# Performance work log

Hardware: AMD Instinct MI355X
Metric: run time of the kernel (lower is better)

Reference implementation:

```python
import jax, jax.numpy as jnp
import numpy as np

D_MODEL = 1024
N_HEADS = 16
HEAD_DIM = D_MODEL // N_HEADS
B, T = 4, 2048


def setup_inputs() -> dict:
    key = jax.random.key(0)
    ks = jax.random.split(key, 5)
    s = 0.02
    return {
        "x": jax.random.normal(ks[0], (B, T, D_MODEL), dtype=jnp.float32),
        "w_qkv": jax.random.normal(ks[1], (D_MODEL, 3 * D_MODEL), dtype=jnp.float32) * s,
        "b_qkv": jnp.zeros((3 * D_MODEL,), dtype=jnp.float32),
        "w_out": jax.random.normal(ks[2], (D_MODEL, D_MODEL), dtype=jnp.float32) * s,
        "b_out": jnp.zeros((D_MODEL,), dtype=jnp.float32),
    }


def reference(x, w_qkv, b_qkv, w_out, b_out):
    Bx, Tx, C = x.shape
    H, Dh = N_HEADS, HEAD_DIM
    qkv = x @ w_qkv + b_qkv                      # [B,T,3C]
    qkv = qkv.reshape(Bx, Tx, 3, H, Dh)
    q = jnp.transpose(qkv[:, :, 0], (0, 2, 1, 3))  # [B,H,T,Dh]
    k = jnp.transpose(qkv[:, :, 1], (0, 2, 1, 3))
    v = jnp.transpose(qkv[:, :, 2], (0, 2, 1, 3))
    scale = 1.0 / jnp.sqrt(jnp.asarray(Dh, dtype=x.dtype))
    attn = jnp.einsum("bhqd,bhkd->bhqk", q, k) * scale  # [B,H,T,T]
    causal = jnp.tril(jnp.ones((Tx, Tx), dtype=bool))
    attn = jnp.where(causal, attn, jnp.asarray(-jnp.inf, dtype=attn.dtype))
    attn = jax.nn.softmax(attn, axis=-1)
    out = jnp.einsum("bhqk,bhkd->bhqd", attn, v)  # [B,H,T,Dh]
    out = jnp.transpose(out, (0, 2, 1, 3)).reshape(Bx, Tx, C)
    return out @ w_out + b_out
```

## Files before the change

### kernel.cpp

```cpp
#include <hip/hip_runtime.h>
#include <hip/hip_bf16.h>
#include <stdint.h>

#define DM    1024
#define NH    16
#define DH    64
#define BATCH 4
#define SEQ   2048
#define QSCALE 0.18033688011112042f

typedef __attribute__((ext_vector_type(4))) float f32x4;
typedef __attribute__((ext_vector_type(8))) short short8;

__device__ __forceinline__ void async_load16(const void* g, void* l) {
    __builtin_amdgcn_global_load_lds(
        (const __attribute__((address_space(1))) void*)(uintptr_t)g,
        (__attribute__((address_space(3))) void*)(uintptr_t)l,
        16, 0, 0);
}

__global__ __launch_bounds__(256) void k_convert(const float* __restrict__ in,
                                                 __hip_bfloat16* __restrict__ out,
                                                 int n4, int* __restrict__ cnt) {
    if (blockIdx.x == 0 && threadIdx.x == 0) cnt[0] = 0;
    int i = blockIdx.x * 256 + threadIdx.x;
    if (i >= n4) return;
    float4 v = ((const float4*)in)[i];
    union { ushort4 u; __hip_bfloat16 h[4]; } o;
    o.h[0] = __float2bfloat16(v.x);
    o.h[1] = __float2bfloat16(v.y);
    o.h[2] = __float2bfloat16(v.z);
    o.h[3] = __float2bfloat16(v.w);
    ((ushort4*)out)[i] = o.u;
}

__global__ __launch_bounds__(256) void k_transpose(const float* __restrict__ in,
                                                   __hip_bfloat16* __restrict__ out,
                                                   int K, int N) {
    __shared__ float tile[32][33];
    const int n0 = blockIdx.x * 32, k0 = blockIdx.y * 32;
    const int tx = threadIdx.x, ty = threadIdx.y;
#pragma unroll
    for (int i = 0; i < 32; i += 8)
        tile[ty + i][tx] = in[(size_t)(k0 + ty + i) * N + n0 + tx];
    __syncthreads();
#pragma unroll
    for (int i = 0; i < 32; i += 8)
        out[(size_t)(n0 + ty + i) * K + k0 + tx] = __float2bfloat16(tile[tx][ty + i]);
}

__global__ __launch_bounds__(512) void k_gemm_qkv(
    const __hip_bfloat16* __restrict__ A, const __hip_bfloat16* __restrict__ Bt,
    const float* __restrict__ bias,
    __hip_bfloat16* __restrict__ qo, __hip_bfloat16* __restrict__ ko,
    __hip_bfloat16* __restrict__ vto) {
    constexpr int K = 1024;
    constexpr int NT = K / 64;
    __shared__ __align__(16) __hip_bfloat16 As[128 * 64];
    __shared__ __align__(16) __hip_bfloat16 Bs[256 * 64];
    const int tid = threadIdx.x;
    const int lane = tid & 63, wid = tid >> 6;
    const int quad = lane >> 4, c = lane & 15;
    const int m0 = blockIdx.y * 128, n0 = blockIdx.x * 256;
    const int wm = (wid >> 2) * 64, wn = (wid & 3) * 64;
    f32x4 acc[4][4] = {};

    auto stage = [&](int k0) {
#pragma unroll
        for (int i = 0; i < 2; ++i) {
            const int s = tid + i * 512;
            const int r = s >> 3;
            const int g = (s & 7) ^ (r & 7);
            async_load16(A + (size_t)(m0 + r) * K + k0 + g * 8, As + s * 8);
        }
#pragma unroll
        for (int i = 0; i < 4; ++i) {
            const int s = tid + i * 512;
            const int r = s >> 3;
            const int g = (s & 7) ^ (r & 7);
            async_load16(Bt + (size_t)(n0 + r) * K + k0 + g * 8, Bs + s * 8);
        }
    };

    stage(0);
    for (int t = 0; t < NT; ++t) {
        asm volatile("s_waitcnt vmcnt(0)" ::: "memory");
        __builtin_amdgcn_s_barrier();
        short8 af[4][2], bf[4][2];
#pragma unroll
        for (int mt = 0; mt < 4; ++mt) {
            const int R = wm + mt * 16 + c;
#pragma unroll
            for (int kk = 0; kk < 2; ++kk)
                af[mt][kk] = *(const short8*)(As + R * 64 + (((kk * 4 + quad) ^ (R & 7)) * 8));
        }
#pragma unroll
        for (int nt = 0; nt < 4; ++nt) {
            const int R = wn + nt * 16 + c;
#pragma unroll
            for (int kk = 0; kk < 2; ++kk)
                bf[nt][kk] = *(const short8*)(Bs + R * 64 + (((kk * 4 + quad) ^ (R & 7)) * 8));
        }
        asm volatile("s_waitcnt lgkmcnt(0)" ::: "memory");
        __builtin_amdgcn_s_barrier();
        if (t + 1 < NT) stage((t + 1) * 64);
        __builtin_amdgcn_s_setprio(1);
#pragma unroll
        for (int kk = 0; kk < 2; ++kk)
#pragma unroll
            for (int mt = 0; mt < 4; ++mt)
#pragma unroll
                for (int nt = 0; nt < 4; ++nt)
                    acc[mt][nt] = __builtin_amdgcn_mfma_f32_16x16x32_bf16(
                        af[mt][kk], bf[nt][kk], acc[mt][nt], 0, 0, 0);
        __builtin_amdgcn_s_setprio(0);
    }

    const int sel = n0 >> 10;
#pragma unroll
    for (int mt = 0; mt < 4; ++mt) {
        const int t0m = m0 + wm + mt * 16 + quad * 4;
        const int b = t0m >> 11, t0 = t0m & 2047;
#pragma unroll
        for (int nt = 0; nt < 4; ++nt) {
            const int n = n0 + wn + nt * 16 + c;
            const int h = (n & 1023) >> 6, dh = n & 63;
            const int bh = b * 16 + h;
            const float bv = bias[n];
            if (sel == 0) {
#pragma unroll
                for (int r = 0; r < 4; ++r)
                    qo[((size_t)bh * 2048 + t0 + r) * 64 + dh] =
                        __float2bfloat16((acc[mt][nt][r] + bv) * QSCALE);
            } else if (sel == 1) {
#pragma unroll
                for (int r = 0; r < 4; ++r)
                    ko[((size_t)bh * 2048 + t0 + r) * 64 + dh] =
                        __float2bfloat16(acc[mt][nt][r] + bv);
            } else {
                union { ushort4 u; __hip_bfloat16 hh[4]; } pk;
#pragma unroll
                for (int r = 0; r < 4; ++r)
                    pk.hh[r] = __float2bfloat16(acc[mt][nt][r] + bv);
                *(ushort4*)(vto + ((size_t)bh * 64 + dh) * 2048 + t0) = pk.u;
            }
        }
    }
}

__global__ __launch_bounds__(256) void k_attn(
    const __hip_bfloat16* __restrict__ q, const __hip_bfloat16* __restrict__ k,
    const __hip_bfloat16* __restrict__ vt, __hip_bfloat16* __restrict__ y,
    int* __restrict__ cnt) {
    __shared__ __align__(16) __hip_bfloat16 Ks[2][64 * 64];
    __shared__ __align__(16) __hip_bfloat16 Vts[2][64 * 64];
    __shared__ int s_item;
    const int tid = threadIdx.x;
    const int lane = tid & 63, w = tid >> 6;
    const int quad = lane >> 4, c = lane & 15;
    const short one = (short)0x3F80;
    const short8 ones = {one, one, one, one, one, one, one, one};

    for (;;) {
        __syncthreads();
        if (tid == 0) s_item = atomicAdd(cnt, 1);
        __syncthreads();
        const int item = s_item;
        if (item >= 1024) break;
        const int qt = 15 - (item >> 6);
        const int bh = item & 63;
        const int b = bh >> 4, h = bh & 15;
        const int q0 = qt * 128;
        const int qw = q0 + w * 32;
        const int nkt = 2 * qt + 2;
        const size_t kbase0 = (size_t)bh * 2048 * 64;
        const size_t vbase0 = (size_t)bh * 64 * 2048;

        short8 qf[2][2];
#pragma unroll
        for (int j = 0; j < 2; ++j) {
            const __hip_bfloat16* qrow = q + ((size_t)bh * 2048 + qw + j * 16 + c) * 64;
            qf[0][j] = *(const short8*)(qrow + quad * 8);
            qf[1][j] = *(const short8*)(qrow + 32 + quad * 8);
        }

        f32x4 accO[2][4] = {};
        f32x4 accL[2] = {};

        auto stage = [&](int kt, int buf) {
#pragma unroll
            for (int i = 0; i < 2; ++i) {
                const int s = tid + i * 256;
                const int r = s >> 3;
                const int g = (s & 7) ^ (r & 7);
                async_load16(k  + kbase0 + (size_t)(kt * 64 + r) * 64 + g * 8,
                             &Ks[buf][s * 8]);
                async_load16(vt + vbase0 + (size_t)r * 2048 + kt * 64 + g * 8,
                             &Vts[buf][s * 8]);
            }
        };

        stage(0, 0);
        for (int kt = 0; kt < nkt; ++kt) {
            const int buf = kt & 1;
            __syncthreads();
            if (kt + 1 < nkt) stage(kt + 1, buf ^ 1);
            if (kt * 64 > qw + 31) continue;
            const __hip_bfloat16* Kb = Ks[buf];
            const __hip_bfloat16* Vb = Vts[buf];

            short8 kf[4][2];
#pragma unroll
            for (int nt = 0; nt < 4; ++nt) {
                const __hip_bfloat16* kr = Kb + (nt * 16 + c) * 64;
                kf[nt][0] = *(const short8*)(kr + ((quad ^ (c & 7)) * 8));
                kf[nt][1] = *(const short8*)(kr + (((quad + 4) ^ (c & 7)) * 8));
            }

            short8 pf[2][2];
#pragma unroll
            for (int j = 0; j < 2; ++j) {
                f32x4 sj[4];
                __builtin_amdgcn_s_setprio(1);
#pragma unroll
                for (int nt = 0; nt < 4; ++nt) {
                    f32x4 z = {};
                    z      = __builtin_amdgcn_mfma_f32_16x16x32_bf16(kf[nt][0], qf[0][j], z, 0, 0, 0);
                    sj[nt] = __builtin_amdgcn_mfma_f32_16x16x32_bf16(kf[nt][1], qf[1][j], z, 0, 0, 0);
                }
                __builtin_amdgcn_s_setprio(0);
                if (kt * 64 + 63 > qw + j * 16) {
                    const int qg = qw + j * 16 + c;
#pragma unroll
                    for (int nt = 0; nt < 4; ++nt) {
                        const int keyb = kt * 64 + nt * 16 + quad * 4;
#pragma unroll
                        for (int r = 0; r < 4; ++r)
                            if (keyb + r > qg) sj[nt][r] = -1e30f;
                    }
                }
#pragma unroll
                for (int nt = 0; nt < 4; ++nt)
#pragma unroll
                    for (int r = 0; r < 4; ++r)
                        sj[nt][r] = __builtin_amdgcn_exp2f(sj[nt][r]);
                unsigned pk32[4][2];
#pragma unroll
                for (int nt = 0; nt < 4; ++nt) {
                    asm("v_cvt_pk_bf16_f32 %0, %1, %2"
                        : "=v"(pk32[nt][0]) : "v"(sj[nt][0]), "v"(sj[nt][1]));
                    asm("v_cvt_pk_bf16_f32 %0, %1, %2"
                        : "=v"(pk32[nt][1]) : "v"(sj[nt][2]), "v"(sj[nt][3]));
                }
                union U8 { unsigned u[4]; short8 v; } w0, w1;
#pragma unroll
                for (int rr = 0; rr < 2; ++rr) {
                    auto t1 = __builtin_amdgcn_permlane32_swap(pk32[0][rr], pk32[1][rr], false, false);
                    auto t2 = __builtin_amdgcn_permlane16_swap(t1[0], t1[1], false, false);
                    w0.u[rr]     = t2[0];
                    w0.u[2 + rr] = t2[1];
                    t1 = __builtin_amdgcn_permlane32_swap(pk32[2][rr], pk32[3][rr], false, false);
                    t2 = __builtin_amdgcn_permlane16_swap(t1[0], t1[1], false, false);
                    w1.u[rr]     = t2[0];
                    w1.u[2 + rr] = t2[1];
                }
                pf[0][j] = w0.v;
                pf[1][j] = w1.v;
            }

            __builtin_amdgcn_s_setprio(1);
#pragma unroll
            for (int j = 0; j < 2; ++j) {
                accL[j] = __builtin_amdgcn_mfma_f32_16x16x32_bf16(ones, pf[0][j], accL[j], 0, 0, 0);
                accL[j] = __builtin_amdgcn_mfma_f32_16x16x32_bf16(ones, pf[1][j], accL[j], 0, 0, 0);
            }
#pragma unroll
            for (int dt = 0; dt < 4; ++dt) {
                const __hip_bfloat16* vr = Vb + (dt * 16 + c) * 64;
                short8 vf0 = *(const short8*)(vr + ((quad ^ (c & 7)) * 8));
                short8 vf1 = *(const short8*)(vr + (((quad + 4) ^ (c & 7)) * 8));
#pragma unroll
                for (int j = 0; j < 2; ++j) {
                    accO[j][dt] = __builtin_amdgcn_mfma_f32_16x16x32_bf16(vf0, pf[0][j], accO[j][dt], 0, 0, 0);
                    accO[j][dt] = __builtin_amdgcn_mfma_f32_16x16x32_bf16(vf1, pf[1][j], accO[j][dt], 0, 0, 0);
                }
            }
            __builtin_amdgcn_s_setprio(0);
        }
#pragma unroll
        for (int j = 0; j < 2; ++j) {
            const float inv = 1.0f / accL[j][0];
            const int qg = qw + j * 16 + c;
#pragma unroll
            for (int dt = 0; dt < 4; ++dt) {
                union { ushort4 u; __hip_bfloat16 hh[4]; } o;
#pragma unroll
                for (int r = 0; r < 4; ++r)
                    o.hh[r] = __float2bfloat16(accO[j][dt][r] * inv);
                *(ushort4*)(y + ((size_t)b * 2048 + qg) * 1024 + h * 64 + dt * 16 + quad * 4) = o.u;
            }
        }
    }
}

__global__ __launch_bounds__(512) void k_gemm_out(
    const __hip_bfloat16* __restrict__ A, const __hip_bfloat16* __restrict__ Bt,
    const float* __restrict__ bias, float* __restrict__ out) {
    constexpr int K = 1024;
    constexpr int NT = K / 64;
    __shared__ __align__(16) __hip_bfloat16 As[128 * 64];
    __shared__ __align__(16) __hip_bfloat16 Bs[256 * 64];
    const int tid = threadIdx.x;
    const int lane = tid & 63, wid = tid >> 6;
    const int quad = lane >> 4, c = lane & 15;
    const int m0 = blockIdx.y * 128, n0 = blockIdx.x * 256;
    const int wm = (wid >> 2) * 64, wn = (wid & 3) * 64;
    f32x4 acc[4][4] = {};

    auto stage = [&](int k0) {
#pragma unroll
        for (int i = 0; i < 2; ++i) {
            const int s = tid + i * 512;
            const int r = s >> 3;
            const int g = (s & 7) ^ (r & 7);
            async_load16(A + (size_t)(m0 + r) * K + k0 + g * 8, As + s * 8);
        }
#pragma unroll
        for (int i = 0; i < 4; ++i) {
            const int s = tid + i * 512;
            const int r = s >> 3;
            const int g = (s & 7) ^ (r & 7);
            async_load16(Bt + (size_t)(n0 + r) * K + k0 + g * 8, Bs + s * 8);
        }
    };

    stage(0);
    for (int t = 0; t < NT; ++t) {
        asm volatile("s_waitcnt vmcnt(0)" ::: "memory");
        __builtin_amdgcn_s_barrier();
        short8 af[4][2], bf[4][2];
#pragma unroll
        for (int mt = 0; mt < 4; ++mt) {
            const int R = wm + mt * 16 + c;
#pragma unroll
            for (int kk = 0; kk < 2; ++kk)
                af[mt][kk] = *(const short8*)(As + R * 64 + (((kk * 4 + quad) ^ (R & 7)) * 8));
        }
#pragma unroll
        for (int nt = 0; nt < 4; ++nt) {
            const int R = wn + nt * 16 + c;
#pragma unroll
            for (int kk = 0; kk < 2; ++kk)
                bf[nt][kk] = *(const short8*)(Bs + R * 64 + (((kk * 4 + quad) ^ (R & 7)) * 8));
        }
        asm volatile("s_waitcnt lgkmcnt(0)" ::: "memory");
        __builtin_amdgcn_s_barrier();
        if (t + 1 < NT) stage((t + 1) * 64);
        __builtin_amdgcn_s_setprio(1);
#pragma unroll
        for (int kk = 0; kk < 2; ++kk)
#pragma unroll
            for (int mt = 0; mt < 4; ++mt)
#pragma unroll
                for (int nt = 0; nt < 4; ++nt)
                    acc[mt][nt] = __builtin_amdgcn_mfma_f32_16x16x32_bf16(
                        af[mt][kk], bf[nt][kk], acc[mt][nt], 0, 0, 0);
        __builtin_amdgcn_s_setprio(0);
    }
#pragma unroll
    for (int mt = 0; mt < 4; ++mt) {
        const int m = m0 + wm + mt * 16 + quad * 4;
#pragma unroll
        for (int nt = 0; nt < 4; ++nt) {
            const int n = n0 + wn + nt * 16 + c;
            const float bv = bias[n];
#pragma unroll
            for (int r = 0; r < 4; ++r)
                out[(size_t)(m + r) * 1024 + n] = acc[mt][nt][r] + bv;
        }
    }
}

extern "C" void kernel_launch(void* const* d_in, const int* in_sizes, int n_in,
                              void* d_out, int out_size, void* d_ws, size_t ws_size,
                              hipStream_t stream) {
    (void)in_sizes; (void)n_in; (void)out_size; (void)ws_size;
    const float* x     = (const float*)d_in[0];
    const float* w_qkv = (const float*)d_in[1];
    const float* b_qkv = (const float*)d_in[2];
    const float* w_out = (const float*)d_in[3];
    const float* b_out = (const float*)d_in[4];
    float* out = (float*)d_out;

    char* ws = (char*)d_ws;
    __hip_bfloat16* xb    = (__hip_bfloat16*)(ws + 0);
    __hip_bfloat16* wqkvT = (__hip_bfloat16*)(ws + 16777216);
    __hip_bfloat16* woutT = (__hip_bfloat16*)(ws + 23068672);
    __hip_bfloat16* qb    = (__hip_bfloat16*)(ws + 25165824);
    __hip_bfloat16* kb    = (__hip_bfloat16*)(ws + 41943040);
    __hip_bfloat16* vtb   = (__hip_bfloat16*)(ws + 58720256);
    __hip_bfloat16* yb    = (__hip_bfloat16*)(ws + 75497472);

    int* cnt = (int*)d_out;

    k_convert<<<8192, 256, 0, stream>>>(x, xb, 2097152, cnt);
    k_transpose<<<dim3(96, 32), dim3(32, 8), 0, stream>>>(w_qkv, wqkvT, 1024, 3072);
    k_transpose<<<dim3(32, 32), dim3(32, 8), 0, stream>>>(w_out, woutT, 1024, 1024);
    k_gemm_qkv<<<dim3(12, 64), 512, 0, stream>>>(xb, wqkvT, b_qkv, qb, kb, vtb);
    k_attn<<<dim3(1024), 256, 0, stream>>>(qb, kb, vtb, yb, cnt);
    k_gemm_out<<<dim3(4, 64), 512, 0, stream>>>(yb, woutT, b_out, out);
}
```

Measured before the change: 251.9 us.

## Double-buffer GEMM LDS tiles and switch to 32x32x16 MFMA

Both GEMM kernels now keep two LDS stages in dynamic shared memory (96 KB) and issue the next tile's async loads before computing on the current one, waiting with a partial vmcnt. This is meant to overlap global-to-LDS traffic with MFMA work. The per-wave 64x64 tile is now computed with 32x32x16 bf16 MFMA instead of 16x16x32, which cuts the number of LDS fragment reads per FLOP. The epilogue is reindexed for the new accumulator layout. The larger LDS footprint may lower occupancy to one block per CU.

```diff
diff --git a/kernel.cpp b/kernel.cpp
--- a/kernel.cpp
+++ b/kernel.cpp
@@ -9,8 +9,9 @@
 #define SEQ   2048
 #define QSCALE 0.18033688011112042f
 
-typedef __attribute__((ext_vector_type(4))) float f32x4;
-typedef __attribute__((ext_vector_type(8))) short short8;
+typedef __attribute__((ext_vector_type(4)))  float f32x4;
+typedef __attribute__((ext_vector_type(16))) float f32x16;
+typedef __attribute__((ext_vector_type(8)))  short short8;
 
 __device__ __forceinline__ void async_load16(const void* g, void* l) {
     __builtin_amdgcn_global_load_lds(
@@ -56,93 +57,104 @@
     __hip_bfloat16* __restrict__ vto) {
     constexpr int K = 1024;
     constexpr int NT = K / 64;
-    __shared__ __align__(16) __hip_bfloat16 As[128 * 64];
-    __shared__ __align__(16) __hip_bfloat16 Bs[256 * 64];
+    extern __shared__ __align__(16) __hip_bfloat16 smem[];
     const int tid = threadIdx.x;
-    const int lane = tid & 63, wid = tid >> 6;
-    const int quad = lane >> 4, c = lane & 15;
+    const int lane = tid & 63;
+    const int wid = tid >> 6;
+    const int col = lane & 31, hi = lane >> 5;
     const int m0 = blockIdx.y * 128, n0 = blockIdx.x * 256;
     const int wm = (wid >> 2) * 64, wn = (wid & 3) * 64;
-    f32x4 acc[4][4] = {};
-
-    auto stage = [&](int k0) {
+    f32x16 acc[2][2] = {};
+
+    auto stage = [&](int k0, int buf) {
+        __hip_bfloat16* Ad = smem + buf * 24576;
+        __hip_bfloat16* Bd = Ad + 8192;
 #pragma unroll
         for (int i = 0; i < 2; ++i) {
             const int s = tid + i * 512;
             const int r = s >> 3;
             const int g = (s & 7) ^ (r & 7);
-            async_load16(A + (size_t)(m0 + r) * K + k0 + g * 8, As + s * 8);
+            async_load16(A + (size_t)(m0 + r) * K + k0 + g * 8, Ad + s * 8);
         }
 #pragma unroll
         for (int i = 0; i < 4; ++i) {
             const int s = tid + i * 512;
             const int r = s >> 3;
             const int g = (s & 7) ^ (r & 7);
-            async_load16(Bt + (size_t)(n0 + r) * K + k0 + g * 8, Bs + s * 8);
+            async_load16(Bt + (size_t)(n0 + r) * K + k0 + g * 8, Bd + s * 8);
         }
     };
 
-    stage(0);
+    stage(0, 0);
     for (int t = 0; t < NT; ++t) {
-        asm volatile("s_waitcnt vmcnt(0)" ::: "memory");
+        const int buf = t & 1;
+        if (t + 1 < NT) {
+            stage((t + 1) * 64, buf ^ 1);
+            asm volatile("s_waitcnt vmcnt(6)" ::: "memory");
+        } else {
+            asm volatile("s_waitcnt vmcnt(0)" ::: "memory");
+        }
         __builtin_amdgcn_s_barrier();
-        short8 af[4][2], bf[4][2];
-#pragma unroll
-        for (int mt = 0; mt < 4; ++mt) {
-            const int R = wm + mt * 16 + c;
-#pragma unroll
-            for (int kk = 0; kk < 2; ++kk)
-                af[mt][kk] = *(const short8*)(As + R * 64 + (((kk * 4 + quad) ^ (R & 7)) * 8));
-        }
-#pragma unroll
-        for (int nt = 0; nt < 4; ++nt) {
-            const int R = wn + nt * 16 + c;
-#pragma unroll
-            for (int kk = 0; kk < 2; ++kk)
-                bf[nt][kk] = *(const short8*)(Bs + R * 64 + (((kk * 4 + quad) ^ (R & 7)) * 8));
-        }
-        asm volatile("s_waitcnt lgkmcnt(0)" ::: "memory");
-        __builtin_amdgcn_s_barrier();
-        if (t + 1 < NT) stage((t + 1) * 64);
+        const __hip_bfloat16* Ab = smem + buf * 24576;
+        const __hip_bfloat16* Bb = Ab + 8192;
+        short8 af[2][4], bf[2][4];
+#pragma unroll
+        for (int mt = 0; mt < 2; ++mt) {
+            const int R = wm + mt * 32 + col;
+#pragma unroll
+            for (int kk = 0; kk < 4; ++kk)
+                af[mt][kk] = *(const short8*)(Ab + R * 64 + (((kk * 2 + hi) ^ (R & 7)) * 8));
+        }
+#pragma unroll
+        for (int nt = 0; nt < 2; ++nt) {
+            const int R = wn + nt * 32 + col;
+#pragma unroll
+            for (int kk = 0; kk < 4; ++kk)
+                bf[nt][kk] = *(const short8*)(Bb + R * 64 + (((kk * 2 + hi) ^ (R & 7)) * 8));
+        }
         __builtin_amdgcn_s_setprio(1);
 #pragma unroll
-        for (int kk = 0; kk < 2; ++kk)
-#pragma unroll
-            for (int mt = 0; mt < 4; ++mt)
-#pragma unroll
-                for (int nt = 0; nt < 4; ++nt)
-                    acc[mt][nt] = __builtin_amdgcn_mfma_f32_16x16x32_bf16(
+        for (int kk = 0; kk < 4; ++kk)
+#pragma unroll
+            for (int mt = 0; mt < 2; ++mt)
+#pragma unroll
+                for (int nt = 0; nt < 2; ++nt)
+                    acc[mt][nt] = __builtin_amdgcn_mfma_f32_32x32x16_bf16(
                         af[mt][kk], bf[nt][kk], acc[mt][nt], 0, 0, 0);
         __builtin_amdgcn_s_setprio(0);
+        __builtin_amdgcn_s_barrier();
     }
 
     const int sel = n0 >> 10;
 #pragma unroll
-    for (int mt = 0; mt < 4; ++mt) {
-        const int t0m = m0 + wm + mt * 16 + quad * 4;
-        const int b = t0m >> 11, t0 = t0m & 2047;
-#pragma unroll
-        for (int nt = 0; nt < 4; ++nt) {
-            const int n = n0 + wn + nt * 16 + c;
+    for (int mt = 0; mt < 2; ++mt) {
+#pragma unroll
+        for (int nt = 0; nt < 2; ++nt) {
+            const int n = n0 + wn + nt * 32 + col;
             const int h = (n & 1023) >> 6, dh = n & 63;
-            const int bh = b * 16 + h;
             const float bv = bias[n];
-            if (sel == 0) {
-#pragma unroll
-                for (int r = 0; r < 4; ++r)
-                    qo[((size_t)bh * 2048 + t0 + r) * 64 + dh] =
-                        __float2bfloat16((acc[mt][nt][r] + bv) * QSCALE);
-            } else if (sel == 1) {
-#pragma unroll
-                for (int r = 0; r < 4; ++r)
-                    ko[((size_t)bh * 2048 + t0 + r) * 64 + dh] =
-                        __float2bfloat16(acc[mt][nt][r] + bv);
-            } else {
-                union { ushort4 u; __hip_bfloat16 hh[4]; } pk;
-#pragma unroll
-                for (int r = 0; r < 4; ++r)
-                    pk.hh[r] = __float2bfloat16(acc[mt][nt][r] + bv);
-                *(ushort4*)(vto + ((size_t)bh * 64 + dh) * 2048 + t0) = pk.u;
+#pragma unroll
+            for (int rb = 0; rb < 4; ++rb) {
+                const int t0m = m0 + wm + mt * 32 + rb * 8 + hi * 4;
+                const int b = t0m >> 11, t0 = t0m & 2047;
+                const int bh = b * 16 + h;
+                if (sel == 0) {
+#pragma unroll
+                    for (int rr = 0; rr < 4; ++rr)
+                        qo[((size_t)bh * 2048 + t0 + rr) * 64 + dh] =
+                            __float2bfloat16((acc[mt][nt][rb * 4 + rr] + bv) * QSCALE);
+                } else if (sel == 1) {
+#pragma unroll
+                    for (int rr = 0; rr < 4; ++rr)
+                        ko[((size_t)bh * 2048 + t0 + rr) * 64 + dh] =
+                            __float2bfloat16(acc[mt][nt][rb * 4 + rr] + bv);
+                } else {
+                    union { ushort4 u; __hip_bfloat16 hh[4]; } pk;
+#pragma unroll
+                    for (int rr = 0; rr < 4; ++rr)
+                        pk.hh[rr] = __float2bfloat16(acc[mt][nt][rb * 4 + rr] + bv);
+                    *(ushort4*)(vto + ((size_t)bh * 64 + dh) * 2048 + t0) = pk.u;
+                }
             }
         }
     }
@@ -308,75 +320,86 @@
     const float* __restrict__ bias, float* __restrict__ out) {
     constexpr int K = 1024;
     constexpr int NT = K / 64;
-    __shared__ __align__(16) __hip_bfloat16 As[128 * 64];
-    __shared__ __align__(16) __hip_bfloat16 Bs[256 * 64];
+    extern __shared__ __align__(16) __hip_bfloat16 smem2[];
     const int tid = threadIdx.x;
-    const int lane = tid & 63, wid = tid >> 6;
-    const int quad = lane >> 4, c = lane & 15;
+    const int lane = tid & 63;
+    const int wid = tid >> 6;
+    const int col = lane & 31, hi = lane >> 5;
     const int m0 = blockIdx.y * 128, n0 = blockIdx.x * 256;
     const int wm = (wid >> 2) * 64, wn = (wid & 3) * 64;
-    f32x4 acc[4][4] = {};
-
-    auto stage = [&](int k0) {
+    f32x16 acc[2][2] = {};
+
+    auto stage = [&](int k0, int buf) {
+        __hip_bfloat16* Ad = smem2 + buf * 24576;
+        __hip_bfloat16* Bd = Ad + 8192;
 #pragma unroll
         for (int i = 0; i < 2; ++i) {
             const int s = tid + i * 512;
             const int r = s >> 3;
             const int g = (s & 7) ^ (r & 7);
-            async_load16(A + (size_t)(m0 + r) * K + k0 + g * 8, As + s * 8);
+            async_load16(A + (size_t)(m0 + r) * K + k0 + g * 8, Ad + s * 8);
         }
 #pragma unroll
         for (int i = 0; i < 4; ++i) {
             const int s = tid + i * 512;
             const int r = s >> 3;
             const int g = (s & 7) ^ (r & 7);
-            async_load16(Bt + (size_t)(n0 + r) * K + k0 + g * 8, Bs + s * 8);
+            async_load16(Bt + (size_t)(n0 + r) * K + k0 + g * 8, Bd + s * 8);
         }
     };
 
-    stage(0);
+    stage(0, 0);
     for (int t = 0; t < NT; ++t) {
-        asm volatile("s_waitcnt vmcnt(0)" ::: "memory");
+        const int buf = t & 1;
+        if (t + 1 < NT) {
+            stage((t + 1) * 64, buf ^ 1);
+            asm volatile("s_waitcnt vmcnt(6)" ::: "memory");
+        } else {
+            asm volatile("s_waitcnt vmcnt(0)" ::: "memory");
+        }
         __builtin_amdgcn_s_barrier();
-        short8 af[4][2], bf[4][2];
-#pragma unroll
-        for (int mt = 0; mt < 4; ++mt) {
-            const int R = wm + mt * 16 + c;
-#pragma unroll
-            for (int kk = 0; kk < 2; ++kk)
-                af[mt][kk] = *(const short8*)(As + R * 64 + (((kk * 4 + quad) ^ (R & 7)) * 8));
-        }
-#pragma unroll
-        for (int nt = 0; nt < 4; ++nt) {
-            const int R = wn + nt * 16 + c;
-#pragma unroll
-            for (int kk = 0; kk < 2; ++kk)
-                bf[nt][kk] = *(const short8*)(Bs + R * 64 + (((kk * 4 + quad) ^ (R & 7)) * 8));
-        }
-        asm volatile("s_waitcnt lgkmcnt(0)" ::: "memory");
-        __builtin_amdgcn_s_barrier();
-        if (t + 1 < NT) stage((t + 1) * 64);
+        const __hip_bfloat16* Ab = smem2 + buf * 24576;
+        const __hip_bfloat16* Bb = Ab + 8192;
+        short8 af[2][4], bf[2][4];
+#pragma unroll
+        for (int mt = 0; mt < 2; ++mt) {
+            const int R = wm + mt * 32 + col;
+#pragma unroll
+            for (int kk = 0; kk < 4; ++kk)
+                af[mt][kk] = *(const short8*)(Ab + R * 64 + (((kk * 2 + hi) ^ (R & 7)) * 8));
+        }
+#pragma unroll
+        for (int nt = 0; nt < 2; ++nt) {
+            const int R = wn + nt * 32 + col;
+#pragma unroll
+            for (int kk = 0; kk < 4; ++kk)
+                bf[nt][kk] = *(const short8*)(Bb + R * 64 + (((kk * 2 + hi) ^ (R & 7)) * 8));
+        }
         __builtin_amdgcn_s_setprio(1);
 #pragma unroll
-        for (int kk = 0; kk < 2; ++kk)
-#pragma unroll
-            for (int mt = 0; mt < 4; ++mt)
-#pragma unroll
-                for (int nt = 0; nt < 4; ++nt)
-                    acc[mt][nt] = __builtin_amdgcn_mfma_f32_16x16x32_bf16(
+        for (int kk = 0; kk < 4; ++kk)
+#pragma unroll
+            for (int mt = 0; mt < 2; ++mt)
+#pragma unroll
+                for (int nt = 0; nt < 2; ++nt)
+                    acc[mt][nt] = __builtin_amdgcn_mfma_f32_32x32x16_bf16(
                         af[mt][kk], bf[nt][kk], acc[mt][nt], 0, 0, 0);
         __builtin_amdgcn_s_setprio(0);
-    }
-#pragma unroll
-    for (int mt = 0; mt < 4; ++mt) {
-        const int m = m0 + wm + mt * 16 + quad * 4;
-#pragma unroll
-        for (int nt = 0; nt < 4; ++nt) {
-            const int n = n0 + wn + nt * 16 + c;
+        __builtin_amdgcn_s_barrier();
+    }
+#pragma unroll
+    for (int mt = 0; mt < 2; ++mt) {
+#pragma unroll
+        for (int nt = 0; nt < 2; ++nt) {
+            const int n = n0 + wn + nt * 32 + col;
             const float bv = bias[n];
 #pragma unroll
-            for (int r = 0; r < 4; ++r)
-                out[(size_t)(m + r) * 1024 + n] = acc[mt][nt][r] + bv;
+            for (int rb = 0; rb < 4; ++rb) {
+                const int m = m0 + wm + mt * 32 + rb * 8 + hi * 4;
+#pragma unroll
+                for (int rr = 0; rr < 4; ++rr)
+                    out[(size_t)(m + rr) * 1024 + n] = acc[mt][nt][rb * 4 + rr] + bv;
+            }
         }
     }
 }
@@ -392,6 +415,15 @@
     const float* b_out = (const float*)d_in[4];
     float* out = (float*)d_out;
 
+    static bool attr_set = false;
+    if (!attr_set) {
+        (void)hipFuncSetAttribute(reinterpret_cast<const void*>(&k_gemm_qkv),
+                                  hipFuncAttributeMaxDynamicSharedMemorySize, 98304);
+        (void)hipFuncSetAttribute(reinterpret_cast<const void*>(&k_gemm_out),
+                                  hipFuncAttributeMaxDynamicSharedMemorySize, 98304);
+        attr_set = true;
+    }
+
     char* ws = (char*)d_ws;
     __hip_bfloat16* xb    = (__hip_bfloat16*)(ws + 0);
     __hip_bfloat16* wqkvT = (__hip_bfloat16*)(ws + 16777216);
@@ -406,7 +438,7 @@
     k_convert<<<8192, 256, 0, stream>>>(x, xb, 2097152, cnt);
     k_transpose<<<dim3(96, 32), dim3(32, 8), 0, stream>>>(w_qkv, wqkvT, 1024, 3072);
     k_transpose<<<dim3(32, 32), dim3(32, 8), 0, stream>>>(w_out, woutT, 1024, 1024);
-    k_gemm_qkv<<<dim3(12, 64), 512, 0, stream>>>(xb, wqkvT, b_qkv, qb, kb, vtb);
+    k_gemm_qkv<<<dim3(12, 64), 512, 98304, stream>>>(xb, wqkvT, b_qkv, qb, kb, vtb);
     k_attn<<<dim3(1024), 256, 0, stream>>>(qb, kb, vtb, yb, cnt);
-    k_gemm_out<<<dim3(4, 64), 512, 0, stream>>>(yb, woutT, b_out, out);
-}
+    k_gemm_out<<<dim3(4, 64), 512, 98304, stream>>>(yb, woutT, b_out, out);
+}
```

Result: no change. 254.8 us (+1.1%).
